# Performance work log

Hardware: AMD Instinct MI355X
Metric: run time of the kernel (lower is better)

The kernel has to match this reference:

```python
import jax, jax.numpy as jnp
import numpy as np

N = 50000   # n_nodes (cells)
E = 800000  # n_edges (avg degree 16)
D = 128     # feature dim


def setup_inputs() -> dict:
    key = jax.random.key(0)
    ks = jax.random.split(key, 8)
    x = jax.random.normal(ks[0], (N, D), dtype=jnp.float32)
    src = jax.random.randint(ks[1], (E,), 0, N, dtype=jnp.int32)
    dst = jax.random.randint(ks[2], (E,), 0, N, dtype=jnp.int32)
    vals = jax.random.uniform(ks[3], (E,), dtype=jnp.float32)
    # GraphConvolution weight (dim -> dim), applied as x @ W
    W_gc = jax.random.normal(ks[4], (D, D), dtype=jnp.float32) / np.sqrt(D).astype(np.float32)
    b_gc = jnp.zeros((D,), jnp.float32)
    # linear2: nn.Linear(dim, dim) -> x @ W2.T + b2
    W2 = jax.random.normal(ks[5], (D, D), dtype=jnp.float32) / np.sqrt(D).astype(np.float32)
    b2 = jnp.zeros((D,), jnp.float32)
    return {"x": x, "vals": vals, "W_gc": W_gc, "b_gc": b_gc,
            "W2": W2, "b2": b2, "src": src, "dst": dst}


def reference(x, vals, W_gc, b_gc, W2, b2, src, dst):
    # GraphConvolution (dropout is identity in eval mode):
    #   support = x @ W + b ; out = relu(adj_sparse @ support)
    support = x @ W_gc + b_gc                         # [N, D]
    msg = support[src] * vals[:, None]                # gather rows, scale by edge weight
    agg = jax.ops.segment_sum(msg, dst, num_segments=N)  # SpMM via scatter-add
    x1 = jax.nn.relu(agg)                             # [N, D]
    # linear2 + dropout(eval=identity) + detached L2 row-normalize
    x2 = x1 @ W2.T + b2                               # [N, D]
    nrm = jax.lax.stop_gradient(
        jnp.sqrt(jnp.sum(x2 * x2, axis=1, keepdims=True)))
    return x2 / nrm
```

## Files before the change

kernel.cpp:

```cpp
#include <hip/hip_runtime.h>
#include <hip/hip_bf16.h>

#define N_NODES 50000
#define N_EDGES 800000
#define DIM     128
#define N_BKT    782
#define CHUNK_E  4096
#define EDGE_CHUNKS 196
#define BCAP     1536
#define EBUF_CAP 1408
#define CONV_BLOCKS 128
#define D1_BLOCKS (EDGE_CHUNKS + CONV_BLOCKS + 16)
#define AGS      68

typedef short short8 __attribute__((ext_vector_type(8)));
typedef float floatx4 __attribute__((ext_vector_type(4)));

__device__ inline unsigned short f2bf(float f) {
    __hip_bfloat16 h = __float2bfloat16(f);
    return *reinterpret_cast<unsigned short*>(&h);
}

__device__ inline uint4 pack8(const float a[8]) {
    uint4 o;
    o.x = (unsigned)f2bf(a[0]) | ((unsigned)f2bf(a[1]) << 16);
    o.y = (unsigned)f2bf(a[2]) | ((unsigned)f2bf(a[3]) << 16);
    o.z = (unsigned)f2bf(a[4]) | ((unsigned)f2bf(a[5]) << 16);
    o.w = (unsigned)f2bf(a[6]) | ((unsigned)f2bf(a[7]) << 16);
    return o;
}

__global__ __launch_bounds__(256) void fused1(
    const float* __restrict__ x, const float* __restrict__ W1,
    const float* __restrict__ W2,
    const int* __restrict__ src, const int* __restrict__ dst,
    const float* __restrict__ vals,
    unsigned int* __restrict__ xb, int* __restrict__ bcnt,
    int2* __restrict__ bucketed,
    uint4* __restrict__ p1, uint4* __restrict__ p2)
{
    __shared__ int bh[800];
    __shared__ int rcur[800];
    const int t = threadIdx.x;

    if (blockIdx.x < EDGE_CHUNKS) {
        const int chunk = blockIdx.x;
        for (int i = t; i < 800; i += 256) bh[i] = 0;
        __syncthreads();
        const int base   = chunk * CHUNK_E;
        const int navail = min(CHUNK_E, N_EDGES - base);
        const int4* d4 = reinterpret_cast<const int4*>(dst + base);
        #pragma unroll
        for (int i = 0; i < 4; ++i) {
            const int j = t + i * 256;
            if (j * 4 < navail) {
                const int4 d = d4[j];
                atomicAdd(&bh[d.x >> 6], 1);
                atomicAdd(&bh[d.y >> 6], 1);
                atomicAdd(&bh[d.z >> 6], 1);
                atomicAdd(&bh[d.w >> 6], 1);
            }
        }
        __syncthreads();
        for (int b = t; b < N_BKT; b += 256)
            rcur[b] = b * BCAP + atomicAdd(&bcnt[b], bh[b]);
        __syncthreads();
        const int4*   s4 = reinterpret_cast<const int4*>(src + base);
        const float4* v4 = reinterpret_cast<const float4*>(vals + base);
        #pragma unroll
        for (int i = 0; i < 4; ++i) {
            const int j = t + i * 256;
            if (j * 4 < navail) {
                const int4   s = s4[j];
                const int4   d = d4[j];
                const float4 v = v4[j];
                int p;
                p = atomicAdd(&rcur[d.x >> 6], 1);
                bucketed[p] = make_int2((s.x & 0xFFFF) | ((d.x & 63) << 16), __float_as_int(v.x));
                p = atomicAdd(&rcur[d.y >> 6], 1);
                bucketed[p] = make_int2((s.y & 0xFFFF) | ((d.y & 63) << 16), __float_as_int(v.y));
                p = atomicAdd(&rcur[d.z >> 6], 1);
                bucketed[p] = make_int2((s.z & 0xFFFF) | ((d.z & 63) << 16), __float_as_int(v.z));
                p = atomicAdd(&rcur[d.w >> 6], 1);
                bucketed[p] = make_int2((s.w & 0xFFFF) | ((d.w & 63) << 16), __float_as_int(v.w));
            }
        }
    } else if (blockIdx.x < EDGE_CHUNKS + CONV_BLOCKS) {
        const int cb = blockIdx.x - EDGE_CHUNKS;
        const float4* x4 = reinterpret_cast<const float4*>(x);
        uint2* xb2 = reinterpret_cast<uint2*>(xb);
        for (int i = cb * 256 + t; i < N_NODES * DIM / 4; i += CONV_BLOCKS * 256) {
            const float4 f = x4[i];
            uint2 o;
            o.x = (unsigned)f2bf(f.x) | ((unsigned)f2bf(f.y) << 16);
            o.y = (unsigned)f2bf(f.z) | ((unsigned)f2bf(f.w) << 16);
            xb2[i] = o;
        }
    } else if (blockIdx.x < EDGE_CHUNKS + CONV_BLOCKS + 8) {
        const int pb   = blockIdx.x - (EDGE_CHUNKS + CONV_BLOCKS);
        const int s    = pb * 256 + t;
        const int lane = s & 63;
        const int nt   = (s >> 6) & 7;
        const int ks   = s >> 9;
        const int m    = lane & 15;
        const int q    = lane >> 4;
        unsigned short e[8];
        #pragma unroll
        for (int j = 0; j < 8; ++j)
            e[j] = f2bf(W1[(ks * 32 + q * 8 + j) * DIM + nt * 16 + m]);
        uint4 o;
        o.x = (unsigned)e[0] | ((unsigned)e[1] << 16);
        o.y = (unsigned)e[2] | ((unsigned)e[3] << 16);
        o.z = (unsigned)e[4] | ((unsigned)e[5] << 16);
        o.w = (unsigned)e[6] | ((unsigned)e[7] << 16);
        p1[s] = o;
    } else {
        const int pb   = blockIdx.x - (EDGE_CHUNKS + CONV_BLOCKS + 8);
        const int s    = pb * 256 + t;
        const int lane = s & 63;
        const int nt   = (s >> 6) & 7;
        const int ks   = s >> 9;
        const int m    = lane & 15;
        const int q    = lane >> 4;
        const float4 f0 = *reinterpret_cast<const float4*>(&W2[(nt * 16 + m) * DIM + ks * 32 + q * 8]);
        const float4 f1 = *reinterpret_cast<const float4*>(&W2[(nt * 16 + m) * DIM + ks * 32 + q * 8 + 4]);
        unsigned short e[8];
        e[0] = f2bf(f0.x); e[1] = f2bf(f0.y); e[2] = f2bf(f0.z); e[3] = f2bf(f0.w);
        e[4] = f2bf(f1.x); e[5] = f2bf(f1.y); e[6] = f2bf(f1.z); e[7] = f2bf(f1.w);
        uint4 o;
        o.x = (unsigned)e[0] | ((unsigned)e[1] << 16);
        o.y = (unsigned)e[2] | ((unsigned)e[3] << 16);
        o.z = (unsigned)e[4] | ((unsigned)e[5] << 16);
        o.w = (unsigned)e[6] | ((unsigned)e[7] << 16);
        p2[s] = o;
    }
}

__global__ __launch_bounds__(512) void agg_gemms(
    const unsigned int* __restrict__ xb, const int2* __restrict__ bucketed,
    const int* __restrict__ bcnt,
    const short8* __restrict__ Bp1, const short8* __restrict__ Bp2,
    const float* __restrict__ bias1, const float* __restrict__ bias2,
    float* __restrict__ out)
{
    __shared__ int2 ebuf[EBUF_CAP];
    __shared__ unsigned int agg[64 * AGS];
    __shared__ float sv[64];
    __shared__ int cnt[64];
    __shared__ int coff[64];
    __shared__ int cur[64];

    const int b = blockIdx.x;
    const int t = threadIdx.x;
    int nE = bcnt[b];
    if (nE > EBUF_CAP) nE = EBUF_CAP;
    const int base = b * BCAP;

    if (t < 64) cnt[t] = 0;
    __syncthreads();
    for (int i = t; i < nE; i += 512)
        atomicAdd(&cnt[(bucketed[base + i].x >> 16) & 63], 1);
    __syncthreads();
    if (t < 64) coff[t] = cnt[t];
    __syncthreads();
    for (int off = 1; off < 64; off <<= 1) {
        int u = 0;
        if (t < 64 && t >= off) u = coff[t - off];
        __syncthreads();
        if (t < 64 && t >= off) coff[t] += u;
        __syncthreads();
    }
    if (t < 64) cur[t] = coff[t] - cnt[t];
    __syncthreads();
    for (int i = t; i < nE; i += 512) {
        const int2 e = bucketed[base + i];
        const int  n = (e.x >> 16) & 63;
        const int  p = atomicAdd(&cur[n], 1);
        ebuf[p] = e;
    }
    __syncthreads();

    const int w    = t >> 6;
    const int lane = t & 63;
    const int g    = lane >> 4;
    const int dl   = lane & 15;

    for (int nl = w * 8; nl < w * 8 + 8; ++nl) {
        const int end = cur[nl];
        const int c   = cnt[nl];
        const int beg = end - c;
        float acc[8];
        #pragma unroll
        for (int k = 0; k < 8; ++k) acc[k] = 0.f;
        float sval = 0.f;

        const int nI = (c + 3) >> 2;
        auto step = [&](int it) {
            const int  idx = beg + it * 4 + g;
            const bool vld = idx < end;
            const int2 e   = ebuf[vld ? idx : beg];
            const float val = vld ? __int_as_float(e.y) : 0.f;
            const uint4 u = *reinterpret_cast<const uint4*>(
                &xb[(size_t)(e.x & 0xFFFF) * 64 + dl * 4]);
            sval += val;
            acc[0] += __uint_as_float(u.x << 16)          * val;
            acc[1] += __uint_as_float(u.x & 0xffff0000u)  * val;
            acc[2] += __uint_as_float(u.y << 16)          * val;
            acc[3] += __uint_as_float(u.y & 0xffff0000u)  * val;
            acc[4] += __uint_as_float(u.z << 16)          * val;
            acc[5] += __uint_as_float(u.z & 0xffff0000u)  * val;
            acc[6] += __uint_as_float(u.w << 16)          * val;
            acc[7] += __uint_as_float(u.w & 0xffff0000u)  * val;
        };
        int it = 0;
        for (; it + 3 < nI; it += 4) { step(it); step(it+1); step(it+2); step(it+3); }
        for (; it < nI; ++it) step(it);

        #pragma unroll
        for (int k = 0; k < 8; ++k) {
            acc[k] += __shfl_xor(acc[k], 16);
            acc[k] += __shfl_xor(acc[k], 32);
        }
        sval += __shfl_xor(sval, 16);
        sval += __shfl_xor(sval, 32);
        if (lane == 0) sv[nl] = sval;
        if (lane < 16) {
            *reinterpret_cast<uint4*>(&agg[nl * AGS + dl * 4]) = pack8(acc);
        }
    }
    __syncthreads();

    const bool act = (w < 4) && (b * 64 + w * 16 < N_NODES);
    const int m = lane & 15;
    const int q = lane >> 4;
    unsigned short* aggs = reinterpret_cast<unsigned short*>(agg);

    if (act) {
        short8 a[4];
        #pragma unroll
        for (int ks = 0; ks < 4; ++ks) {
            const uint4 t4 = *reinterpret_cast<const uint4*>(&agg[(w * 16 + m) * AGS + ks * 16 + q * 4]);
            a[ks] = *reinterpret_cast<const short8*>(&t4);
        }
        floatx4 acc[8];
        #pragma unroll
        for (int nt = 0; nt < 8; ++nt) { acc[nt][0]=0.f; acc[nt][1]=0.f; acc[nt][2]=0.f; acc[nt][3]=0.f; }
        #pragma unroll
        for (int ks = 0; ks < 4; ++ks) {
            #pragma unroll
            for (int nt = 0; nt < 8; ++nt) {
                const short8 bf = Bp1[(ks * 8 + nt) * 64 + lane];
                acc[nt] = __builtin_amdgcn_mfma_f32_16x16x32_bf16(a[ks], bf, acc[nt], 0, 0, 0);
            }
        }
        float sv4[4];
        #pragma unroll
        for (int i = 0; i < 4; ++i) sv4[i] = sv[w * 16 + q * 4 + i];
        #pragma unroll
        for (int nt = 0; nt < 8; ++nt) {
            const float bb = bias1[nt * 16 + m];
            #pragma unroll
            for (int i = 0; i < 4; ++i) {
                const float v = fmaxf(acc[nt][i] + sv4[i] * bb, 0.f);
                aggs[(w * 16 + q * 4 + i) * (AGS * 2) + nt * 16 + m] = f2bf(v);
            }
        }
    }
    __syncthreads();

    if (!act) return;
    const int row0 = b * 64 + w * 16;

    short8 a[4];
    #pragma unroll
    for (int ks = 0; ks < 4; ++ks) {
        const uint4 t4 = *reinterpret_cast<const uint4*>(&aggs[(w * 16 + m) * (AGS * 2) + ks * 32 + q * 8]);
        a[ks] = *reinterpret_cast<const short8*>(&t4);
    }

    floatx4 acc[8];
    #pragma unroll
    for (int nt = 0; nt < 8; ++nt) { acc[nt][0]=0.f; acc[nt][1]=0.f; acc[nt][2]=0.f; acc[nt][3]=0.f; }

    #pragma unroll
    for (int ks = 0; ks < 4; ++ks) {
        #pragma unroll
        for (int nt = 0; nt < 8; ++nt) {
            const short8 bf = Bp2[(ks * 8 + nt) * 64 + lane];
            acc[nt] = __builtin_amdgcn_mfma_f32_16x16x32_bf16(a[ks], bf, acc[nt], 0, 0, 0);
        }
    }

    #pragma unroll
    for (int nt = 0; nt < 8; ++nt) {
        const float bb = bias2[nt * 16 + m];
        #pragma unroll
        for (int i = 0; i < 4; ++i) acc[nt][i] += bb;
    }

    float sq[4] = {0.f, 0.f, 0.f, 0.f};
    #pragma unroll
    for (int nt = 0; nt < 8; ++nt)
        #pragma unroll
        for (int i = 0; i < 4; ++i) sq[i] += acc[nt][i] * acc[nt][i];
    #pragma unroll
    for (int i = 0; i < 4; ++i) {
        #pragma unroll
        for (int mask = 1; mask < 16; mask <<= 1)
            sq[i] += __shfl_xor(sq[i], mask);
        sq[i] = 1.0f / sqrtf(sq[i]);
    }

    #pragma unroll
    for (int nt = 0; nt < 8; ++nt) {
        #pragma unroll
        for (int i = 0; i < 4; ++i) {
            const int r = row0 + q * 4 + i;
            out[(size_t)r * DIM + nt * 16 + m] = acc[nt][i] * sq[i];
        }
    }
}

extern "C" void kernel_launch(void* const* d_in, const int* in_sizes, int n_in,
                              void* d_out, int out_size, void* d_ws, size_t ws_size,
                              hipStream_t stream) {
    const float* x    = (const float*)d_in[0];
    const float* vals = (const float*)d_in[1];
    const float* W_gc = (const float*)d_in[2];
    const float* b_gc = (const float*)d_in[3];
    const float* W2   = (const float*)d_in[4];
    const float* b2   = (const float*)d_in[5];
    const int*   src  = (const int*)d_in[6];
    const int*   dst  = (const int*)d_in[7];

    float* out = (float*)d_out;

    const size_t XB_B  = (size_t)N_NODES * DIM * 2;
    const size_t BUK_B = (size_t)N_BKT * BCAP * 8;
    char* wsb = (char*)d_ws;
    unsigned int* xb = (unsigned int*)wsb;
    int2*  bucketed = (int2*)(wsb + XB_B);
    int*   bcnt     = (int*)(wsb + XB_B + BUK_B);
    uint4* pw1      = (uint4*)(wsb + XB_B + BUK_B + 4096);
    uint4* pw2      = (uint4*)(wsb + XB_B + BUK_B + 4096 + 32768);

    hipMemsetAsync(bcnt, 0, 800 * sizeof(int), stream);

    fused1<<<D1_BLOCKS, 256, 0, stream>>>(
        x, W_gc, W2, src, dst, vals, xb, bcnt, bucketed, pw1, pw2);

    agg_gemms<<<N_BKT, 512, 0, stream>>>(
        xb, bucketed, bcnt, (const short8*)pw1, (const short8*)pw2,
        b_gc, b2, out);
}
```

Baseline: 153.7 us.

## Stage bucketed edges in shared memory for coalesced global scatter

Edge-chunk blocks now compute a local prefix sum over the bucket histogram, scatter edges into a shared-memory buffer sorted by bucket, and then write them to global memory in contiguous runs per bucket. This replaces random per-edge global writes with mostly sequential ones. The conversion block count is also raised from 128 to 224. The cost is a larger shared-memory footprint (about 32KB for the edge buffer plus 16KB of tables), which lowers occupancy for every role in the fused kernel, and extra barriers for the scan.

```diff
diff --git a/kernel.cpp b/kernel.cpp
--- a/kernel.cpp
+++ b/kernel.cpp
@@ -9,7 +9,7 @@
 #define EDGE_CHUNKS 196
 #define BCAP     1536
 #define EBUF_CAP 1408
-#define CONV_BLOCKS 128
+#define CONV_BLOCKS 224
 #define D1_BLOCKS (EDGE_CHUNKS + CONV_BLOCKS + 16)
 #define AGS      68
 
@@ -39,51 +39,85 @@
     int2* __restrict__ bucketed,
     uint4* __restrict__ p1, uint4* __restrict__ p2)
 {
-    __shared__ int bh[800];
-    __shared__ int rcur[800];
+    __shared__ __align__(16) int2 ebuf[CHUNK_E];
+    __shared__ int hist[1024];
+    __shared__ int lstart[1024];
+    __shared__ int gbase[1024];
+    __shared__ int lcur[1024];
+    __shared__ int tsum[256];
     const int t = threadIdx.x;
 
     if (blockIdx.x < EDGE_CHUNKS) {
         const int chunk = blockIdx.x;
-        for (int i = t; i < 800; i += 256) bh[i] = 0;
-        __syncthreads();
-        const int base   = chunk * CHUNK_E;
-        const int navail = min(CHUNK_E, N_EDGES - base);
+        const int base  = chunk * CHUNK_E;
+        const int nav   = min(CHUNK_E, N_EDGES - base);
+        for (int i = t; i < 1024; i += 256) hist[i] = 0;
+        __syncthreads();
+
         const int4* d4 = reinterpret_cast<const int4*>(dst + base);
         #pragma unroll
         for (int i = 0; i < 4; ++i) {
             const int j = t + i * 256;
-            if (j * 4 < navail) {
+            if (j * 4 < nav) {
                 const int4 d = d4[j];
-                atomicAdd(&bh[d.x >> 6], 1);
-                atomicAdd(&bh[d.y >> 6], 1);
-                atomicAdd(&bh[d.z >> 6], 1);
-                atomicAdd(&bh[d.w >> 6], 1);
+                atomicAdd(&hist[d.x >> 6], 1);
+                atomicAdd(&hist[d.y >> 6], 1);
+                atomicAdd(&hist[d.z >> 6], 1);
+                atomicAdd(&hist[d.w >> 6], 1);
             }
         }
         __syncthreads();
+
+        const int h0 = hist[4*t], h1 = hist[4*t+1], h2 = hist[4*t+2], h3 = hist[4*t+3];
+        const int s  = h0 + h1 + h2 + h3;
+        tsum[t] = s;
+        __syncthreads();
+        for (int off = 1; off < 256; off <<= 1) {
+            int u = 0;
+            if (t >= off) u = tsum[t - off];
+            __syncthreads();
+            if (t >= off) tsum[t] += u;
+            __syncthreads();
+        }
+        const int ex = tsum[t] - s;
+        lstart[4*t]   = ex;
+        lstart[4*t+1] = ex + h0;
+        lstart[4*t+2] = ex + h0 + h1;
+        lstart[4*t+3] = ex + h0 + h1 + h2;
+        lcur[4*t]   = ex;
+        lcur[4*t+1] = ex + h0;
+        lcur[4*t+2] = ex + h0 + h1;
+        lcur[4*t+3] = ex + h0 + h1 + h2;
         for (int b = t; b < N_BKT; b += 256)
-            rcur[b] = b * BCAP + atomicAdd(&bcnt[b], bh[b]);
-        __syncthreads();
+            gbase[b] = b * BCAP + atomicAdd(&bcnt[b], hist[b]);
+        __syncthreads();
+
         const int4*   s4 = reinterpret_cast<const int4*>(src + base);
         const float4* v4 = reinterpret_cast<const float4*>(vals + base);
         #pragma unroll
         for (int i = 0; i < 4; ++i) {
             const int j = t + i * 256;
-            if (j * 4 < navail) {
-                const int4   s = s4[j];
-                const int4   d = d4[j];
-                const float4 v = v4[j];
-                int p;
-                p = atomicAdd(&rcur[d.x >> 6], 1);
-                bucketed[p] = make_int2((s.x & 0xFFFF) | ((d.x & 63) << 16), __float_as_int(v.x));
-                p = atomicAdd(&rcur[d.y >> 6], 1);
-                bucketed[p] = make_int2((s.y & 0xFFFF) | ((d.y & 63) << 16), __float_as_int(v.y));
-                p = atomicAdd(&rcur[d.z >> 6], 1);
-                bucketed[p] = make_int2((s.z & 0xFFFF) | ((d.z & 63) << 16), __float_as_int(v.z));
-                p = atomicAdd(&rcur[d.w >> 6], 1);
-                bucketed[p] = make_int2((s.w & 0xFFFF) | ((d.w & 63) << 16), __float_as_int(v.w));
+            if (j * 4 < nav) {
+                const int4   sw = s4[j];
+                const int4   dw = d4[j];
+                const float4 vw = v4[j];
+                int b, p;
+                b = dw.x >> 6; p = atomicAdd(&lcur[b], 1);
+                ebuf[p] = make_int2((sw.x & 0xFFFF) | ((dw.x & 63) << 16) | (b << 22), __float_as_int(vw.x));
+                b = dw.y >> 6; p = atomicAdd(&lcur[b], 1);
+                ebuf[p] = make_int2((sw.y & 0xFFFF) | ((dw.y & 63) << 16) | (b << 22), __float_as_int(vw.y));
+                b = dw.z >> 6; p = atomicAdd(&lcur[b], 1);
+                ebuf[p] = make_int2((sw.z & 0xFFFF) | ((dw.z & 63) << 16) | (b << 22), __float_as_int(vw.z));
+                b = dw.w >> 6; p = atomicAdd(&lcur[b], 1);
+                ebuf[p] = make_int2((sw.w & 0xFFFF) | ((dw.w & 63) << 16) | (b << 22), __float_as_int(vw.w));
             }
+        }
+        __syncthreads();
+
+        for (int i = t; i < nav; i += 256) {
+            const int2 e = ebuf[i];
+            const int  b = ((unsigned)e.x) >> 22;
+            bucketed[gbase[b] + (i - lstart[b])] = make_int2(e.x & 0x3FFFFF, e.y);
         }
     } else if (blockIdx.x < EDGE_CHUNKS + CONV_BLOCKS) {
         const int cb = blockIdx.x - EDGE_CHUNKS;
@@ -98,10 +132,10 @@
         }
     } else if (blockIdx.x < EDGE_CHUNKS + CONV_BLOCKS + 8) {
         const int pb   = blockIdx.x - (EDGE_CHUNKS + CONV_BLOCKS);
-        const int s    = pb * 256 + t;
-        const int lane = s & 63;
-        const int nt   = (s >> 6) & 7;
-        const int ks   = s >> 9;
+        const int sI   = pb * 256 + t;
+        const int lane = sI & 63;
+        const int nt   = (sI >> 6) & 7;
+        const int ks   = sI >> 9;
         const int m    = lane & 15;
         const int q    = lane >> 4;
         unsigned short e[8];
@@ -113,13 +147,13 @@
         o.y = (unsigned)e[2] | ((unsigned)e[3] << 16);
         o.z = (unsigned)e[4] | ((unsigned)e[5] << 16);
         o.w = (unsigned)e[6] | ((unsigned)e[7] << 16);
-        p1[s] = o;
+        p1[sI] = o;
     } else {
         const int pb   = blockIdx.x - (EDGE_CHUNKS + CONV_BLOCKS + 8);
-        const int s    = pb * 256 + t;
-        const int lane = s & 63;
-        const int nt   = (s >> 6) & 7;
-        const int ks   = s >> 9;
+        const int sI   = pb * 256 + t;
+        const int lane = sI & 63;
+        const int nt   = (sI >> 6) & 7;
+        const int ks   = sI >> 9;
         const int m    = lane & 15;
         const int q    = lane >> 4;
         const float4 f0 = *reinterpret_cast<const float4*>(&W2[(nt * 16 + m) * DIM + ks * 32 + q * 8]);
@@ -132,7 +166,7 @@
         o.y = (unsigned)e[2] | ((unsigned)e[3] << 16);
         o.z = (unsigned)e[4] | ((unsigned)e[5] << 16);
         o.w = (unsigned)e[6] | ((unsigned)e[7] << 16);
-        p2[s] = o;
+        p2[sI] = o;
     }
 }
 
```

Measured after the change: 150.2 us. 2.2% less time.
